# Kernel optimization log

Measured on AMD Instinct MI355X. Metric: run time of the kernel, lower is better.

The kernel has to match this reference:

```python
import jax, jax.numpy as jnp
import numpy as np

B, N, G, H = 64, 1000, 500, 256
TANH_CLIP = 10.0


def setup_inputs() -> dict:
    key = jax.random.key(0)
    ks = jax.random.split(key, 8)
    embeddings = jax.random.normal(ks[0], (B, N, H), dtype=jnp.float32)
    dists = jax.random.uniform(ks[1], (B, N, N), dtype=jnp.float32)
    last_node = jax.random.randint(ks[2], (B, G), 0, N)
    visited = jax.random.uniform(ks[3], (B, G, N)) < 0.3
    group_ninf_mask = jnp.where(visited, -jnp.inf, 0.0).astype(jnp.float32)
    s = 1.0 / np.sqrt(H)
    Wq_graph = jax.random.normal(ks[4], (H, H), dtype=jnp.float32) * s
    Wq_first = jax.random.normal(ks[5], (H, H), dtype=jnp.float32) * s
    Wq_last = jax.random.normal(ks[6], (H, H), dtype=jnp.float32) * s
    W_visited = jax.random.normal(ks[7], (H, H), dtype=jnp.float32) * s
    return dict(embeddings=embeddings, dists=dists, last_node=last_node,
                group_ninf_mask=group_ninf_mask, Wq_graph=Wq_graph,
                Wq_first=Wq_first, Wq_last=Wq_last, W_visited=W_visited)


def reference(embeddings, dists, last_node, group_ninf_mask,
              Wq_graph, Wq_first, Wq_last, W_visited) -> jnp.ndarray:
    b, n, h = embeddings.shape
    g = last_node.shape[1]
    inv_sqrt_h = 1.0 / np.float32(np.sqrt(h))
    inv_sqrt_2 = np.float32(1.0 / np.sqrt(2.0))

    # reset(): graph query from mean-pooled embeddings  [B,1,H]
    q_graph = jnp.einsum('bih,oh->bio', embeddings.mean(axis=1, keepdims=True), Wq_graph)

    # gather last-node embeddings  [B,G,H]
    idx = jnp.broadcast_to(last_node[:, :, None], (b, g, h))
    last_emb = jnp.take_along_axis(embeddings, idx, axis=1)
    q_last = jnp.einsum('bgh,oh->bgo', last_emb, Wq_last)
    # first call: q_first built from the same last-node embedding
    q_first = jnp.einsum('bgh,oh->bgo', last_emb, Wq_first)

    # visited-set query: mask (-inf->1) @ embeddings / N, then linear
    mask_visited = jnp.where(jnp.isneginf(group_ninf_mask), 1.0, group_ninf_mask)
    pooled = jnp.einsum('bgn,bnh->bgh', mask_visited, embeddings) / np.float32(n)
    q_visited = jnp.einsum('bgh,oh->bgo', pooled, W_visited)

    # distances from last node to all nodes  [B,G,N]
    didx = jnp.broadcast_to(last_node[:, :, None], (b, g, n))
    distances = jnp.take_along_axis(dists, didx, axis=1)

    final_q = q_last + q_first + q_graph + q_visited  # [B,G,H]
    score = jnp.einsum('bgh,bnh->bgn', final_q, embeddings) * inv_sqrt_h - distances * inv_sqrt_2
    score_clipped = TANH_CLIP * jnp.tanh(score)
    mask_prob = jnp.where(jnp.isneginf(group_ninf_mask), -1e8, group_ninf_mask)
    return jax.nn.softmax(score_clipped + mask_prob, axis=-1)
```

## Files before the change

### kernel.cpp

```cpp
#include <hip/hip_runtime.h>
#include <hip/hip_fp16.h>
#include <math.h>

#define Bb 64
#define Nn 1000
#define Gg 500
#define Hh 256
#define GP 512
#define NP 1024

#define WS_MP   0u
#define WS_QG   16384u
#define WS_RS   32768u
#define WS_BM   65536u
#define WS_WC16 1114112u
#define WS_E16  1179648u
#define WS_T16  9371648u
#define WS_P16  17760256u
#define WS_F16  WS_T16
#define WS_PO   21954560u

typedef __attribute__((ext_vector_type(8))) short short8;
typedef __attribute__((ext_vector_type(8))) _Float16 f16x8;
typedef __attribute__((ext_vector_type(4))) float f32x4;
typedef __attribute__((ext_vector_type(4))) unsigned short u16x4;

#define MFMAH(a,b,c) __builtin_amdgcn_mfma_f32_16x16x32_f16(a,b,c,0,0,0)
#define SW(row, chunk) (((row) << 6) + ((((chunk) ^ ((row) & 7))) << 3))

__device__ __forceinline__ unsigned short f16b(float v) {
  return __half_as_ushort(__float2half(v));
}

__global__ __launch_bounds__(256) void k_zero(float* __restrict__ ws) {
  int bid = blockIdx.x, t = threadIdx.x;
  if (bid < 64) ws[WS_MP + bid * 256 + t] = 0.f;
  else          ws[WS_RS + (bid - 64) * 256 + t] = 0.f;
}

__global__ __launch_bounds__(256) void k_prep(const float* __restrict__ emb,
                                              float* __restrict__ ws) {
  __shared__ float tile[64][68];
  __shared__ float colsum[16][64];
  int nt = blockIdx.x, ht = blockIdx.y, b = blockIdx.z;
  int t = threadIdx.x;
  int c4 = (t & 15) * 4, r0 = t >> 4;
  int n0 = nt * 64, h0 = ht * 64;
  unsigned short* e16 = (unsigned short*)(ws + WS_E16);
  unsigned short* t16 = (unsigned short*)(ws + WS_T16);
  float cs0 = 0.f, cs1 = 0.f, cs2 = 0.f, cs3 = 0.f;
#pragma unroll
  for (int rr = 0; rr < 4; ++rr) {
    int r = r0 + rr * 16;
    int n = n0 + r;
    float4 v = {0.f, 0.f, 0.f, 0.f};
    if (n < Nn) {
      size_t idx = ((size_t)(b * Nn + n)) * Hh + h0 + c4;
      v = *(const float4*)(emb + idx);
      u16x4 e4 = { f16b(v.x), f16b(v.y), f16b(v.z), f16b(v.w) };
      *(u16x4*)(e16 + idx) = e4;
    }
    *(float4*)&tile[r][c4] = v;
    cs0 += v.x; cs1 += v.y; cs2 += v.z; cs3 += v.w;
  }
  colsum[r0][c4 + 0] = cs0; colsum[r0][c4 + 1] = cs1;
  colsum[r0][c4 + 2] = cs2; colsum[r0][c4 + 3] = cs3;
  __syncthreads();
  {
    int h_l = t >> 2, nseg = t & 3;
    short8 h8a, h8b;
#pragma unroll
    for (int i = 0; i < 16; ++i) {
      float v = tile[nseg * 16 + i][h_l];
      unsigned short hv = f16b(v);
      if (i < 8) h8a[i] = (short)hv;
      else       h8b[i-8] = (short)hv;
    }
    size_t base = ((size_t)(b * Hh + h0 + h_l)) * NP + n0 + nseg * 16;
    *(short8*)(t16 + base) = h8a; *(short8*)(t16 + base + 8) = h8b;
  }
  if (t < 64) {
    float s = 0.f;
#pragma unroll
    for (int i = 0; i < 16; ++i) s += colsum[i][t];
    atomicAdd(ws + WS_MP + b * Hh + h0 + t, s);
  }
}

__global__ __launch_bounds__(256) void k_qgraph(const float* __restrict__ Wg,
                                                float* __restrict__ ws) {
  __shared__ float mean[Hh];
  int b = blockIdx.x, t = threadIdx.x;
  mean[t] = ws[WS_MP + b*Hh + t] * (1.0f/Nn);
  __syncthreads();
  const float4* wrow = (const float4*)(Wg + (size_t)t * Hh);
  float acc = 0.f;
#pragma unroll
  for (int h4 = 0; h4 < Hh/4; ++h4) {
    float4 w = wrow[h4];
    acc += mean[h4*4]*w.x + mean[h4*4+1]*w.y + mean[h4*4+2]*w.z + mean[h4*4+3]*w.w;
  }
  ws[WS_QG + b*Hh + t] = acc;
}

__global__ __launch_bounds__(256) void k_wcat(const float* __restrict__ Wf,
                                              const float* __restrict__ Wl,
                                              const float* __restrict__ Wv,
                                              float* __restrict__ ws) {
  int o = blockIdx.x, k = threadIdx.x;
  unsigned short* wc = (unsigned short*)(ws + WS_WC16);
  wc[o*512 + k]       = f16b(Wv[o*Hh + k]);
  wc[o*512 + 256 + k] = f16b(Wl[o*Hh + k] + Wf[o*Hh + k]);
}

__global__ __launch_bounds__(256) void k_bm(const float* __restrict__ gm,
                                            float* __restrict__ ws) {
  int w = threadIdx.x >> 6, l = threadIdx.x & 63;
  int row = blockIdx.x * 4 + w;
  int b = row >> 9, g = row & 511;
  unsigned long long* dst = (unsigned long long*)((unsigned short*)(ws + WS_BM) + (size_t)row * 64);
  if (g < Gg) {
    const float* src = gm + ((size_t)b * Gg + g) * Nn;
#pragma unroll
    for (int i = 0; i < 16; ++i) {
      int n = i * 64 + l;
      bool bit = (n < Nn) ? (src[n] < -1e30f) : false;
      unsigned long long m = __ballot(bit);
      if (l == i) dst[i] = m;
    }
  } else {
    if (l < 16) dst[l] = 0ull;
  }
}

__global__ __launch_bounds__(256, 2) void k_pool(float* __restrict__ ws) {
  __shared__ __align__(16) unsigned short sT[128*64];
  int ht = blockIdx.x, gt = blockIdx.y, b = blockIdx.z;
  int t = threadIdx.x, w = t >> 6, lane = t & 63;
  int wh = w >> 1, wg = w & 1, l15 = lane & 15, lk = lane >> 4;
  const unsigned short* t16 = (const unsigned short*)(ws + WS_T16);
  const unsigned short* bmp = (const unsigned short*)(ws + WS_BM);
  unsigned short* p16 = (unsigned short*)(ws + WS_P16);
  int h0 = ht*128, g0 = gt*128;
  f32x4 acc[4][4] = {};
  const unsigned short* brow[4];
#pragma unroll
  for (int fn = 0; fn < 4; ++fn) {
    int g = g0 + wg*64 + fn*16 + l15; if (g > Gg-1) g = Gg-1;
    brow[fn] = bmp + ((size_t)(b*GP + g)) * 64;
  }
  int bitoff = (lk & 1) * 8;
  int srow = t >> 1, sc0 = (t & 1) * 4;
  size_t sbase = ((size_t)(b*Hh + h0 + srow)) * NP;
  for (int st = 0; st < 16; ++st) {
    int k0 = st * 64;
#pragma unroll
    for (int i = 0; i < 4; ++i) {
      int cc = sc0 + i;
      *(short8*)&sT[SW(srow, cc)] = *(const short8*)(t16 + sbase + k0 + cc*8);
    }
    __syncthreads();
#pragma unroll
    for (int kk = 0; kk < 64; kk += 32) {
      f16x8 ah[4], bmf[4];
#pragma unroll
      for (int fm = 0; fm < 4; ++fm)
        ah[fm] = *(const f16x8*)&sT[SW(wh*64 + fm*16 + l15, (kk>>3) + lk)];
#pragma unroll
      for (int fn = 0; fn < 4; ++fn) {
        unsigned c = brow[fn][((k0 + kk) >> 4) + (lk >> 1)];
        short8 bs;
#pragma unroll
        for (int i = 0; i < 8; ++i)
          bs[i] = ((c >> (bitoff + i)) & 1) ? (short)0x3C00 : (short)0;
        bmf[fn] = *(const f16x8*)&bs;
      }
#pragma unroll
      for (int fm = 0; fm < 4; ++fm)
#pragma unroll
        for (int fn = 0; fn < 4; ++fn)
          acc[fm][fn] = MFMAH(ah[fm], bmf[fn], acc[fm][fn]);
    }
    __syncthreads();
  }
#pragma unroll
  for (int fm = 0; fm < 4; ++fm)
#pragma unroll
    for (int fn = 0; fn < 4; ++fn) {
      int h = h0 + wh*64 + fm*16 + lk*4;
      int g = g0 + wg*64 + fn*16 + l15;
      u16x4 v4;
#pragma unroll
      for (int j = 0; j < 4; ++j) v4[j] = f16b(acc[fm][fn][j] * (1.0f/Nn));
      *(u16x4*)(p16 + ((size_t)(b*GP + g)) * Hh + h) = v4;
    }
}

__global__ __launch_bounds__(256, 2) void k_finalq(const int* __restrict__ last_node,
                                                   float* __restrict__ ws) {
  __shared__ __align__(16) unsigned short sA[128*64], sB[128*64];
  __shared__ int lL[128];
  int ot = blockIdx.x, gt = blockIdx.y, b = blockIdx.z;
  int t = threadIdx.x, w = t >> 6, lane = t & 63;
  int wo = w >> 1, wg = w & 1, l15 = lane & 15, lk = lane >> 4;
  const unsigned short* wc = (const unsigned short*)(ws + WS_WC16);
  const unsigned short* p16 = (const unsigned short*)(ws + WS_P16);
  const unsigned short* e16 = (const unsigned short*)(ws + WS_E16);
  unsigned short* f16 = (unsigned short*)(ws + WS_F16);
  int o0 = ot*128, g0 = gt*128;
  if (t < 128) lL[t] = last_node[b*Gg + ((g0 + t) < Gg ? (g0 + t) : Gg-1)];
  __syncthreads();
  f32x4 acc[4][4] = {};
  int srow = t >> 1, sc0 = (t & 1) * 4;
  size_t abase = ((size_t)(o0 + srow)) * 512;
  size_t pbase = ((size_t)(b*GP + g0 + srow)) * Hh;
  size_t lbase = ((size_t)(b*Nn + lL[srow])) * Hh;
  for (int st = 0; st < 8; ++st) {
    int k0 = st * 64;
#pragma unroll
    for (int i = 0; i < 4; ++i) {
      int cc = sc0 + i;
      int d = SW(srow, cc);
      *(short8*)&sA[d] = *(const short8*)(wc + abase + k0 + cc*8);
      if (k0 < 256)
        *(short8*)&sB[d] = *(const short8*)(p16 + pbase + k0 + cc*8);
      else
        *(short8*)&sB[d] = *(const short8*)(e16 + lbase + (k0 - 256) + cc*8);
    }
    __syncthreads();
#pragma unroll
    for (int kk = 0; kk < 64; kk += 32) {
      f16x8 a[4], bb[4];
#pragma unroll
      for (int fm = 0; fm < 4; ++fm)
        a[fm] = *(const f16x8*)&sA[SW(wo*64 + fm*16 + l15, (kk>>3) + lk)];
#pragma unroll
      for (int fn = 0; fn < 4; ++fn)
        bb[fn] = *(const f16x8*)&sB[SW(wg*64 + fn*16 + l15, (kk>>3) + lk)];
#pragma unroll
      for (int fm = 0; fm < 4; ++fm)
#pragma unroll
        for (int fn = 0; fn < 4; ++fn)
          acc[fm][fn] = MFMAH(a[fm], bb[fn], acc[fm][fn]);
    }
    __syncthreads();
  }
#pragma unroll
  for (int fm = 0; fm < 4; ++fm) {
    int o = o0 + wo*64 + fm*16 + lk*4;
    float4 qv = *(const float4*)(ws + WS_QG + b*Hh + o);
    float q4[4] = {qv.x, qv.y, qv.z, qv.w};
#pragma unroll
    for (int fn = 0; fn < 4; ++fn) {
      int g = g0 + wg*64 + fn*16 + l15;
      u16x4 v4;
#pragma unroll
      for (int j = 0; j < 4; ++j) v4[j] = f16b(acc[fm][fn][j] + q4[j]);
      *(u16x4*)(f16 + ((size_t)(b*GP + g)) * Hh + o) = v4;
    }
  }
}

__global__ __launch_bounds__(256, 4) void k_score(const float* __restrict__ dists,
                                                  const int* __restrict__ last_node,
                                                  float* __restrict__ ws) {
  __shared__ __align__(16) unsigned short sE[128*64], sF[128*64];
  __shared__ int lL[128];
  int gt = blockIdx.x, nt = blockIdx.y, b = blockIdx.z;
  int t = threadIdx.x, w = t >> 6, lane = t & 63;
  int wn = w >> 1, wg = w & 1, l15 = lane & 15, lk = lane >> 4;
  const unsigned short* e16 = (const unsigned short*)(ws + WS_E16);
  const unsigned short* f16 = (const unsigned short*)(ws + WS_F16);
  const unsigned short* bmp = (const unsigned short*)(ws + WS_BM);
  unsigned short* po = (unsigned short*)(ws + WS_PO);
  float* rs = ws + WS_RS;
  int n0 = nt*128, g0 = gt*128;
  if (t < 128) lL[t] = last_node[b*Gg + ((g0 + t) < Gg ? (g0 + t) : Gg-1)];
  __syncthreads();
  f32x4 acc[4][4] = {};
  int srow = t >> 1, sc0 = (t & 1) * 4;
  int nr = n0 + srow; if (nr > Nn-1) nr = Nn-1;
  size_t ebase = ((size_t)(b*Nn + nr)) * Hh;
  size_t fbase = ((size_t)(b*GP + g0 + srow)) * Hh;
  for (int st = 0; st < 4; ++st) {
    int k0 = st * 64;
#pragma unroll
    for (int i = 0; i < 4; ++i) {
      int cc = sc0 + i;
      int d = SW(srow, cc);
      *(short8*)&sE[d] = *(const short8*)(e16 + ebase + k0 + cc*8);
      *(short8*)&sF[d] = *(const short8*)(f16 + fbase + k0 + cc*8);
    }
    __syncthreads();
#pragma unroll
    for (int kk = 0; kk < 64; kk += 32) {
      f16x8 a[4], bb[4];
#pragma unroll
      for (int fm = 0; fm < 4; ++fm)
        a[fm] = *(const f16x8*)&sE[SW(wn*64 + fm*16 + l15, (kk>>3) + lk)];
#pragma unroll
      for (int fn = 0; fn < 4; ++fn)
        bb[fn] = *(const f16x8*)&sF[SW(wg*64 + fn*16 + l15, (kk>>3) + lk)];
#pragma unroll
      for (int fm = 0; fm < 4; ++fm)
#pragma unroll
        for (int fn = 0; fn < 4; ++fn)
          acc[fm][fn] = MFMAH(a[fm], bb[fn], acc[fm][fn]);
    }
    __syncthreads();
  }
  const float c2 = 0.70710678118654752f;
  float rsum[4] = {0.f, 0.f, 0.f, 0.f};
#pragma unroll
  for (int fn = 0; fn < 4; ++fn) {
    int gl = wg*64 + fn*16 + l15;
    int g = g0 + gl;
    if (g < Gg) {
      int L = lL[gl];
      const float* drow = dists + ((size_t)(b*Nn + L)) * Nn;
      const unsigned short* bmr = bmp + ((size_t)(b*GP + g)) * 64;
      unsigned short* prow = po + ((size_t)(b*Gg + g)) * 1024;
#pragma unroll
      for (int fm = 0; fm < 4; ++fm) {
        int n = n0 + wn*64 + fm*16 + lk*4;
        if (n < Nn) {
          float4 d4 = *(const float4*)(drow + n);
          unsigned cb = bmr[n >> 4];
          int bo = n & 15;
          float dd[4] = {d4.x, d4.y, d4.z, d4.w};
          unsigned short h4[4];
#pragma unroll
          for (int j = 0; j < 4; ++j) {
            float s = fmaf(acc[fm][fn][j], 0.0625f, -dd[j] * c2);
            float e = __expf(-2.0f * fabsf(s));
            float r = __builtin_amdgcn_rcpf(1.0f + e);
            float m = fmaf(-20.0f, e * r, 10.0f);
            float parg = copysignf(m, s) - 10.0f;
            float p = ((cb >> (bo + j)) & 1) ? 0.f : __expf(parg);
            rsum[fn] += p;
            h4[j] = f16b(p);
          }
          uint2 u = { (unsigned)h4[0] | ((unsigned)h4[1] << 16),
                      (unsigned)h4[2] | ((unsigned)h4[3] << 16) };
          *(uint2*)(prow + n) = u;
        }
      }
    }
  }
#pragma unroll
  for (int fn = 0; fn < 4; ++fn) {
    rsum[fn] += __shfl_xor(rsum[fn], 16);
    rsum[fn] += __shfl_xor(rsum[fn], 32);
    int g = g0 + wg*64 + fn*16 + l15;
    if (lk == 0 && g < Gg) atomicAdd(rs + b*GP + g, rsum[fn]);
  }
}

__global__ __launch_bounds__(256) void k_norm(const float* __restrict__ ws,
                                              float* __restrict__ out) {
  int idx = blockIdx.x * 256 + threadIdx.x;
  int bg = idx / 125;
  int n = (idx - bg * 125) * 8;
  int b = bg / Gg, g = bg - b * Gg;
  const unsigned short* po = (const unsigned short*)(ws + WS_PO);
  float inv = 1.0f / ws[WS_RS + b*GP + g];
  uint4 u = *(const uint4*)(po + (size_t)bg * 1024 + n);
  float* orow = out + (size_t)bg * Nn + n;
  float4 o0, o1;
  o0.x = __half2float(__ushort_as_half((unsigned short)(u.x & 0xFFFF))) * inv;
  o0.y = __half2float(__ushort_as_half((unsigned short)(u.x >> 16))) * inv;
  o0.z = __half2float(__ushort_as_half((unsigned short)(u.y & 0xFFFF))) * inv;
  o0.w = __half2float(__ushort_as_half((unsigned short)(u.y >> 16))) * inv;
  o1.x = __half2float(__ushort_as_half((unsigned short)(u.z & 0xFFFF))) * inv;
  o1.y = __half2float(__ushort_as_half((unsigned short)(u.z >> 16))) * inv;
  o1.z = __half2float(__ushort_as_half((unsigned short)(u.w & 0xFFFF))) * inv;
  o1.w = __half2float(__ushort_as_half((unsigned short)(u.w >> 16))) * inv;
  *(float4*)orow = o0;
  *(float4*)(orow + 4) = o1;
}

extern "C" void kernel_launch(void* const* d_in, const int* in_sizes, int n_in,
                              void* d_out, int out_size, void* d_ws, size_t ws_size,
                              hipStream_t stream) {
  const float* emb       = (const float*)d_in[0];
  const float* dists     = (const float*)d_in[1];
  const int*   last_node = (const int*)d_in[2];
  const float* gm        = (const float*)d_in[3];
  const float* Wg        = (const float*)d_in[4];
  const float* Wf        = (const float*)d_in[5];
  const float* Wl        = (const float*)d_in[6];
  const float* Wv        = (const float*)d_in[7];
  float* out = (float*)d_out;
  float* ws  = (float*)d_ws;

  hipLaunchKernelGGL(k_zero,   dim3(192),       dim3(256), 0, stream, ws);
  hipLaunchKernelGGL(k_prep,   dim3(16,4,Bb),   dim3(256), 0, stream, emb, ws);
  hipLaunchKernelGGL(k_qgraph, dim3(Bb),        dim3(256), 0, stream, Wg, ws);
  hipLaunchKernelGGL(k_wcat,   dim3(256),       dim3(256), 0, stream, Wf, Wl, Wv, ws);
  hipLaunchKernelGGL(k_bm,     dim3(Bb*GP/4),   dim3(256), 0, stream, gm, ws);
  hipLaunchKernelGGL(k_pool,   dim3(2,4,Bb),    dim3(256), 0, stream, ws);
  hipLaunchKernelGGL(k_finalq, dim3(2,4,Bb),    dim3(256), 0, stream, last_node, ws);
  hipLaunchKernelGGL(k_score,  dim3(4,8,Bb),    dim3(256), 0, stream, dists, last_node, ws);
  hipLaunchKernelGGL(k_norm,   dim3(15625),     dim3(256), 0, stream, ws, out);
}
```

Before: 321.3 us.

## Merge small prep kernels, replace mean atomics with partials, swizzle score grid

Folds the zeroing, mask-bitmap and weight-concat kernels into one launch, removing two kernel launches. The mean-pool column sums are now written as per-tile partials and reduced in k_qgraph instead of using atomicAdd, so the MP buffer no longer needs zeroing. The score kernel switches to a 1D grid with a swizzled block-to-tile mapping that spreads consecutive blocks across batches, which may change L2 and channel locality. The extra workspace region for partials increases workspace usage.

Result: faster. 304.1 us (-5.4%).

```diff
diff --git a/kernel.cpp b/kernel.cpp
--- a/kernel.cpp
+++ b/kernel.cpp
@@ -9,16 +9,16 @@
 #define GP 512
 #define NP 1024
 
-#define WS_MP   0u
-#define WS_QG   16384u
-#define WS_RS   32768u
-#define WS_BM   65536u
-#define WS_WC16 1114112u
-#define WS_E16  1179648u
-#define WS_T16  9371648u
-#define WS_P16  17760256u
+#define WS_QG   0u
+#define WS_RS   16384u
+#define WS_BM   49152u
+#define WS_WC16 1097728u
+#define WS_E16  1163264u
+#define WS_T16  9355264u
+#define WS_P16  17743872u
 #define WS_F16  WS_T16
-#define WS_PO   21954560u
+#define WS_PO   21938176u
+#define WS_MP   38322176u
 
 typedef __attribute__((ext_vector_type(8))) short short8;
 typedef __attribute__((ext_vector_type(8))) _Float16 f16x8;
@@ -32,10 +32,37 @@
   return __half_as_ushort(__float2half(v));
 }
 
-__global__ __launch_bounds__(256) void k_zero(float* __restrict__ ws) {
+__global__ __launch_bounds__(256) void k_misc(const float* __restrict__ gm,
+                                              const float* __restrict__ Wf,
+                                              const float* __restrict__ Wl,
+                                              const float* __restrict__ Wv,
+                                              float* __restrict__ ws) {
   int bid = blockIdx.x, t = threadIdx.x;
-  if (bid < 64) ws[WS_MP + bid * 256 + t] = 0.f;
-  else          ws[WS_RS + (bid - 64) * 256 + t] = 0.f;
+  if (bid < 8192) {
+    int w = t >> 6, l = t & 63;
+    int row = bid * 4 + w;
+    int b = row >> 9, g = row & 511;
+    unsigned long long* dst = (unsigned long long*)((unsigned short*)(ws + WS_BM) + (size_t)row * 64);
+    if (g < Gg) {
+      const float* src = gm + ((size_t)b * Gg + g) * Nn;
+#pragma unroll
+      for (int i = 0; i < 16; ++i) {
+        int n = i * 64 + l;
+        bool bit = (n < Nn) ? (src[n] < -1e30f) : false;
+        unsigned long long m = __ballot(bit);
+        if (l == i) dst[i] = m;
+      }
+    } else {
+      if (l < 16) dst[l] = 0ull;
+    }
+  } else if (bid < 8448) {
+    int o = bid - 8192, k = t;
+    unsigned short* wc = (unsigned short*)(ws + WS_WC16);
+    wc[o*512 + k]       = f16b(Wv[o*Hh + k]);
+    wc[o*512 + 256 + k] = f16b(Wl[o*Hh + k] + Wf[o*Hh + k]);
+  } else {
+    ws[WS_RS + (bid - 8448) * 256 + t] = 0.f;
+  }
 }
 
 __global__ __launch_bounds__(256) void k_prep(const float* __restrict__ emb,
@@ -83,7 +110,7 @@
     float s = 0.f;
 #pragma unroll
     for (int i = 0; i < 16; ++i) s += colsum[i][t];
-    atomicAdd(ws + WS_MP + b * Hh + h0 + t, s);
+    ws[WS_MP + (((size_t)(b * Hh + h0 + t)) << 4) + nt] = s;
   }
 }
 
@@ -91,7 +118,16 @@
                                                 float* __restrict__ ws) {
   __shared__ float mean[Hh];
   int b = blockIdx.x, t = threadIdx.x;
-  mean[t] = ws[WS_MP + b*Hh + t] * (1.0f/Nn);
+  {
+    const float4* mp4 = (const float4*)(ws + WS_MP + (((size_t)(b * Hh + t)) << 4));
+    float s = 0.f;
+#pragma unroll
+    for (int q = 0; q < 4; ++q) {
+      float4 v = mp4[q];
+      s += v.x + v.y + v.z + v.w;
+    }
+    mean[t] = s * (1.0f/Nn);
+  }
   __syncthreads();
   const float4* wrow = (const float4*)(Wg + (size_t)t * Hh);
   float acc = 0.f;
@@ -101,36 +137,6 @@
     acc += mean[h4*4]*w.x + mean[h4*4+1]*w.y + mean[h4*4+2]*w.z + mean[h4*4+3]*w.w;
   }
   ws[WS_QG + b*Hh + t] = acc;
-}
-
-__global__ __launch_bounds__(256) void k_wcat(const float* __restrict__ Wf,
-                                              const float* __restrict__ Wl,
-                                              const float* __restrict__ Wv,
-                                              float* __restrict__ ws) {
-  int o = blockIdx.x, k = threadIdx.x;
-  unsigned short* wc = (unsigned short*)(ws + WS_WC16);
-  wc[o*512 + k]       = f16b(Wv[o*Hh + k]);
-  wc[o*512 + 256 + k] = f16b(Wl[o*Hh + k] + Wf[o*Hh + k]);
-}
-
-__global__ __launch_bounds__(256) void k_bm(const float* __restrict__ gm,
-                                            float* __restrict__ ws) {
-  int w = threadIdx.x >> 6, l = threadIdx.x & 63;
-  int row = blockIdx.x * 4 + w;
-  int b = row >> 9, g = row & 511;
-  unsigned long long* dst = (unsigned long long*)((unsigned short*)(ws + WS_BM) + (size_t)row * 64);
-  if (g < Gg) {
-    const float* src = gm + ((size_t)b * Gg + g) * Nn;
-#pragma unroll
-    for (int i = 0; i < 16; ++i) {
-      int n = i * 64 + l;
-      bool bit = (n < Nn) ? (src[n] < -1e30f) : false;
-      unsigned long long m = __ballot(bit);
-      if (l == i) dst[i] = m;
-    }
-  } else {
-    if (l < 16) dst[l] = 0ull;
-  }
 }
 
 __global__ __launch_bounds__(256, 2) void k_pool(float* __restrict__ ws) {
@@ -266,7 +272,9 @@
                                                   float* __restrict__ ws) {
   __shared__ __align__(16) unsigned short sE[128*64], sF[128*64];
   __shared__ int lL[128];
-  int gt = blockIdx.x, nt = blockIdx.y, b = blockIdx.z;
+  int id = blockIdx.x;
+  int swz = ((id & 7) << 8) | (id >> 3);
+  int gt = swz & 3, nt = (swz >> 2) & 7, b = swz >> 5;
   int t = threadIdx.x, w = t >> 6, lane = t & 63;
   int wn = w >> 1, wg = w & 1, l15 = lane & 15, lk = lane >> 4;
   const unsigned short* e16 = (const unsigned short*)(ws + WS_E16);
@@ -393,13 +401,11 @@
   float* out = (float*)d_out;
   float* ws  = (float*)d_ws;
 
-  hipLaunchKernelGGL(k_zero,   dim3(192),       dim3(256), 0, stream, ws);
+  hipLaunchKernelGGL(k_misc,   dim3(8576),      dim3(256), 0, stream, gm, Wf, Wl, Wv, ws);
   hipLaunchKernelGGL(k_prep,   dim3(16,4,Bb),   dim3(256), 0, stream, emb, ws);
   hipLaunchKernelGGL(k_qgraph, dim3(Bb),        dim3(256), 0, stream, Wg, ws);
-  hipLaunchKernelGGL(k_wcat,   dim3(256),       dim3(256), 0, stream, Wf, Wl, Wv, ws);
-  hipLaunchKernelGGL(k_bm,     dim3(Bb*GP/4),   dim3(256), 0, stream, gm, ws);
   hipLaunchKernelGGL(k_pool,   dim3(2,4,Bb),    dim3(256), 0, stream, ws);
   hipLaunchKernelGGL(k_finalq, dim3(2,4,Bb),    dim3(256), 0, stream, last_node, ws);
-  hipLaunchKernelGGL(k_score,  dim3(4,8,Bb),    dim3(256), 0, stream, dists, last_node, ws);
+  hipLaunchKernelGGL(k_score,  dim3(2048),      dim3(256), 0, stream, dists, last_node, ws);
   hipLaunchKernelGGL(k_norm,   dim3(15625),     dim3(256), 0, stream, ws, out);
 }
```
